# Kernel optimization log

Hardware: AMD Instinct MI355X
Metric: run time of the kernel (lower is better)

Reference implementation:

```python
import jax, jax.numpy as jnp
import numpy as np

N_QUBITS = 9
N_LAYERS = 4
EPS = 1e-5


def _apply_ry(state, wire, theta):
    # state: [N, 2**n] real; theta: [N] or scalar
    n = N_QUBITS
    N = state.shape[0]
    left, right = 2 ** wire, 2 ** (n - 1 - wire)
    s = state.reshape(N, left, 2, right)
    th = jnp.broadcast_to(jnp.asarray(theta, state.dtype), (N,))[:, None, None]
    c, si = jnp.cos(th / 2), jnp.sin(th / 2)
    a, b = s[:, :, 0, :], s[:, :, 1, :]
    out = jnp.stack([c * a - si * b, si * a + c * b], axis=2)
    return out.reshape(N, -1)


def _apply_cnot(state, ctrl, tgt):
    n = N_QUBITS
    N = state.shape[0]
    s = state.reshape((N,) + (2,) * n)
    ca, ta = ctrl + 1, tgt + 1
    sub = jnp.take(s, 1, axis=ca)          # control == 1 slice
    ta2 = ta - 1 if ta > ca else ta
    sub = jnp.flip(sub, axis=ta2)          # X on target
    idx = [slice(None)] * (n + 1)
    idx[ca] = 1
    s = s.at[tuple(idx)].set(sub)
    return s.reshape(N, -1)


def quantum_layer(inputs, q_weights):
    # inputs: [N, n_qubits] angles; q_weights: [n_layers, n_qubits]
    N = inputs.shape[0]
    state = jnp.zeros((N, 2 ** N_QUBITS), inputs.dtype).at[:, 0].set(1.0)
    for i in range(N_QUBITS):
        state = _apply_ry(state, i, inputs[:, i])
    for j in range(N_LAYERS):
        for i in range(N_QUBITS):
            state = _apply_cnot(state, i, (i + 1) % N_QUBITS)
        for i in range(N_QUBITS):
            state = _apply_ry(state, i, q_weights[j, i])
    probs = (state * state).reshape((N,) + (2,) * N_QUBITS)
    zs = []
    for i in range(N_QUBITS):
        axes = tuple(a for a in range(1, N_QUBITS + 1) if a != i + 1)
        p = probs.sum(axes)                # [N, 2]
        zs.append(p[:, 0] - p[:, 1])
    return jnp.stack(zs, axis=1)           # [N, n_qubits]


def _bn(x):
    mu = x.mean((0, 2, 3), keepdims=True)
    var = x.var((0, 2, 3), keepdims=True)
    return (x - mu) * jax.lax.rsqrt(var + EPS)


def _maxpool(x, kh, kw):
    return jax.lax.reduce_window(x, -jnp.inf, jax.lax.max,
                                 (1, 1, kh, kw), (1, 1, kh, kw), 'VALID')


def _conv(x, w):
    return jax.lax.conv_general_dilated(x, w, (1, 1), 'VALID',
                                        dimension_numbers=('NCHW', 'OIHW', 'NCHW'))


def _forward(x, w_conv1, w_conv2, w_conv3, q_weights, fc_w, fc_b):
    h = jax.nn.elu(_bn(_conv(x, w_conv1)))
    h = jnp.pad(h, ((0, 0), (0, 0), (0, 1), (16, 17)))     # ZeroPad2d(16,17,0,1)
    h = _maxpool(jax.nn.elu(_bn(_conv(h, w_conv2))), 2, 4)
    h = jnp.pad(h, ((0, 0), (0, 0), (4, 3), (2, 1)))       # ZeroPad2d(2,1,4,3)
    h = _maxpool(jax.nn.elu(_bn(_conv(h, w_conv3))), 2, 4)
    B, C = h.shape[0], h.shape[1]
    feats = h.reshape(B, C, -1)                            # [B, 32, 9]
    q = quantum_layer(feats.reshape(B * C, N_QUBITS), q_weights)
    q = q.reshape(B, C * N_QUBITS)                         # channel-major concat
    return q @ fc_w.T + fc_b


def setup_inputs() -> dict:
    key = jax.random.key(0)
    ks = jax.random.split(key, 7)
    return {
        'x': jax.random.normal(ks[0], (1024, 1, 4, 216), jnp.float32),
        'w_conv1': jax.random.normal(ks[1], (16, 1, 1, 64), jnp.float32) * 0.05,
        'w_conv2': jax.random.normal(ks[2], (32, 16, 2, 32), jnp.float32) * 0.05,
        'w_conv3': jax.random.normal(ks[3], (32, 32, 8, 4), jnp.float32) * 0.05,
        'q_weights': jax.random.uniform(ks[4], (N_LAYERS, N_QUBITS), jnp.float32, 0.0, 2 * np.pi),
        'fc_w': jax.random.normal(ks[5], (5, 32 * N_QUBITS), jnp.float32) * 0.05,
        'fc_b': jnp.zeros((5,), jnp.float32),
    }


def reference(x, w_conv1, w_conv2, w_conv3, q_weights, fc_w, fc_b):
    return _forward(x, w_conv1, w_conv2, w_conv3, q_weights, fc_w, fc_b)
```

## Files before the change

kernel.cpp:

```cpp
#include <hip/hip_runtime.h>
#include <math.h>

#define NB 1024
#define C1 16
#define H1 4
#define W1 153
#define WX 216
#define K1 64
#define C2 32
#define H2 4
#define W2 155
#define W192 192
#define PW2 38
#define C3 32
#define W3 38

typedef short short4v __attribute__((ext_vector_type(4)));
typedef short short8 __attribute__((ext_vector_type(8)));
typedef float f32x16 __attribute__((ext_vector_type(16)));

#define OFF_OUT1     0
#define OFF_A1H      10027008
#define OFF_A1L      16318464
#define OFF_W2PH     22609920
#define OFF_W2PL     22626304
#define OFF_W3PH     22642688
#define OFF_W3PL     22659072
#define OFF_UH       22675456
#define OFF_UL       22806528
#define OFF_POOL2RAW 22937600
#define OFF_A2H      25427968
#define OFF_A2L      27787264
#define OFF_FEATSRAW 30146560
#define OFF_QO       30441472
#define OFF_PART1    30736384
#define OFF_PART2    30867456
#define OFF_PART3    30998528
#define OFF_STATS1   31031296
#define OFF_STATS2   31031328
#define OFF_STATS3   31031392

__device__ __forceinline__ float eluf(float x){ return x > 0.f ? x : expm1f(x); }

__device__ __forceinline__ ushort bf16h(float x){
  unsigned u = __float_as_uint(x);
  unsigned r = u + 0x7fffu + ((u >> 16) & 1u);
  return (ushort)(r >> 16);
}
__device__ __forceinline__ float bf16f(ushort h){ return __uint_as_float(((unsigned)h) << 16); }

__device__ __forceinline__ short8 cat8(short4v a, short4v b){
  return __builtin_shufflevector(a, b, 0,1,2,3,4,5,6,7);
}

__global__ __launch_bounds__(256) void k_conv1s(const float* __restrict__ x,
                                                const float* __restrict__ w1,
                                                float* __restrict__ out1,
                                                float* __restrict__ part1){
  __shared__ float xr[4][WX];
  __shared__ float wl[C1*K1];
  int n = blockIdx.x, tid = threadIdx.x;
  for (int i = tid; i < 4*WX; i += 256) xr[i/WX][i%WX] = x[(size_t)n*4*WX + i];
  for (int i = tid; i < C1*K1; i += 256) wl[i] = w1[i];
  __syncthreads();
  int h = tid >> 6, lane = tid & 63;
  float acc[16][3];
  #pragma unroll
  for (int c = 0; c < 16; ++c){ acc[c][0]=0.f; acc[c][1]=0.f; acc[c][2]=0.f; }
  bool v2 = (lane + 128) < W1;
  for (int k = 0; k < 64; ++k){
    float x0 = xr[h][lane + k];
    float x1 = xr[h][lane + 64 + k];
    float x2 = v2 ? xr[h][lane + 128 + k] : 0.f;
    #pragma unroll
    for (int c = 0; c < 16; ++c){
      float wk = wl[c*64 + k];
      acc[c][0] += wk*x0; acc[c][1] += wk*x1; acc[c][2] += wk*x2;
    }
  }
  float ss[16], sq[16];
  #pragma unroll
  for (int c = 0; c < 16; ++c){
    float* ob = out1 + (((size_t)(n*16 + c)*4 + h))*W1;
    ob[lane] = acc[c][0];
    ob[lane + 64] = acc[c][1];
    if (v2) ob[lane + 128] = acc[c][2];
    ss[c] = acc[c][0] + acc[c][1] + acc[c][2];
    sq[c] = acc[c][0]*acc[c][0] + acc[c][1]*acc[c][1] + acc[c][2]*acc[c][2];
  }
  #pragma unroll
  for (int m = 1; m < 64; m <<= 1){
    #pragma unroll
    for (int c = 0; c < 16; ++c){ ss[c] += __shfl_xor(ss[c], m); sq[c] += __shfl_xor(sq[c], m); }
  }
  if (lane == 0){
    #pragma unroll
    for (int c = 0; c < 16; ++c){
      part1[((size_t)(n*4 + h)*16 + c)*2]     = ss[c];
      part1[((size_t)(n*4 + h)*16 + c)*2 + 1] = sq[c];
    }
  }
}

__global__ __launch_bounds__(256) void k_stats_finP(const float* __restrict__ part,
                                                    float* __restrict__ stats,
                                                    int C, int nblk, float inv){
  __shared__ float rs[256], rq[256];
  int c = blockIdx.x;
  float s = 0.f, q = 0.f;
  for (int b = threadIdx.x; b < nblk; b += 256){
    s += part[((size_t)b*C + c)*2];
    q += part[((size_t)b*C + c)*2 + 1];
  }
  rs[threadIdx.x] = s; rq[threadIdx.x] = q; __syncthreads();
  for (int st = 128; st > 0; st >>= 1){
    if (threadIdx.x < st){ rs[threadIdx.x] += rs[threadIdx.x+st]; rq[threadIdx.x] += rq[threadIdx.x+st]; }
    __syncthreads();
  }
  if (threadIdx.x == 0){
    float mean = rs[0]*inv;
    float var  = rq[0]*inv - mean*mean;
    stats[c*2]   = mean;
    stats[c*2+1] = rsqrtf(var + 1e-5f);
  }
}

__global__ __launch_bounds__(256) void k_bnelu1(const float* __restrict__ out1,
                                                const float* __restrict__ stats,
                                                ushort* __restrict__ a1h, ushort* __restrict__ a1l){
  __shared__ float xf[2448];
  __shared__ float st[32];
  int b = blockIdx.x;
  int n = b >> 2, h = b & 3;
  int tid = threadIdx.x;
  if (tid < 32) st[tid] = stats[tid];
  for (int i = tid; i < 2448; i += 256){
    int ci = i / 153, w = i - ci*153;
    xf[i] = out1[((size_t)(n*16 + ci)*4 + h)*W1 + w];
  }
  __syncthreads();
  for (int i = tid; i < 3072; i += 256){
    int w = i >> 4, ci = i & 15;
    float v = 0.f;
    int ws = w - 16;
    if ((unsigned)ws < (unsigned)W1){
      float xx = xf[ci*153 + ws];
      v = eluf((xx - st[ci*2])*st[ci*2+1]);
    }
    int ciS = ci ^ (((w >> 2) & 1) << 3);
    size_t o = (size_t)b*3072 + w*16 + ciS;
    ushort hs = bf16h(v);
    a1h[o] = hs;
    a1l[o] = bf16h(v - bf16f(hs));
  }
}

__global__ void k_cvtw(const float* __restrict__ w2, const float* __restrict__ w3,
                       ushort* __restrict__ w2ph, ushort* __restrict__ w2pl,
                       ushort* __restrict__ w3ph, ushort* __restrict__ w3pl){
  int idx = blockIdx.x*256 + threadIdx.x;
  if (idx < 32768){
    int ci = idx & 15; int co = (idx >> 4) & 31; int rk = idx >> 9;
    int r = rk >> 5, kw = rk & 31;
    float v = w2[((size_t)(co*16 + ci)*2 + r)*32 + kw];
    ushort hs = bf16h(v); float hf = bf16f(hs);
    w2ph[idx] = hs; w2pl[idx] = bf16h(v - hf);
  } else {
    int j = idx - 32768;
    int ci = j & 31; int co = (j >> 5) & 31; int rk = j >> 10;
    int r = rk >> 2, kw = rk & 3;
    float v = w3[((size_t)(co*32 + ci)*8 + r)*4 + kw];
    ushort hs = bf16h(v); float hf = bf16f(hs);
    w3ph[j] = hs; w3pl[j] = bf16h(v - hf);
  }
}

template<int HG, int PS>
__device__ __forceinline__ void conv2_body(const ushort* s_hi, const ushort* s_lo,
                                           const ushort* __restrict__ w2ph,
                                           const ushort* __restrict__ w2pl,
                                           float* __restrict__ pool2raw,
                                           float (*statW)[32][2],
                                           int n, int l31, int l5){
  constexpr int P0 = (PS == 0) ? 0 : (PS + 1);
  constexpr int NP = (PS == 0) ? 2 : 1;
  constexpr int NR = (HG == 0) ? 3 : 2;
  int e8 = l5*8;

  f32x16 acc[2][NP];
  #pragma unroll
  for (int lh = 0; lh < 2; ++lh)
    #pragma unroll
    for (int p = 0; p < NP; ++p)
      #pragma unroll
      for (int e = 0; e < 16; ++e) acc[lh][p][e] = 0.f;

  for (int kw = 0; kw < 32; ++kw){
    short8 Ah[2], Al[2];
    #pragma unroll
    for (int r = 0; r < 2; ++r){
      int widx = ((r*32 + kw)*32 + l31)*16 + e8;
      Ah[r] = *(const short8*)(w2ph + widx);
      Al[r] = *(const short8*)(w2pl + widx);
    }
    #pragma unroll
    for (int j = 0; j < NR; ++j){
      int rb = j*3072;
      short8 bh[NP], bl[NP];
      #pragma unroll
      for (int p = 0; p < NP; ++p){
        int pos = (P0 + p)*32 + l31 + kw;
        int off = rb + pos*16 + (e8 ^ (((pos >> 2) & 1) << 3));
        bh[p] = *(const short8*)(s_hi + off);
        bl[p] = *(const short8*)(s_lo + off);
      }
      #pragma unroll
      for (int lh = 0; lh < 2; ++lh){
        #pragma unroll
        for (int r = 0; r < 2; ++r){
          if (lh + r != j) continue;
          #pragma unroll
          for (int p = 0; p < NP; ++p){
            acc[lh][p] = __builtin_amdgcn_mfma_f32_32x32x16_bf16(Ah[r], bh[p], acc[lh][p], 0, 0, 0);
            acc[lh][p] = __builtin_amdgcn_mfma_f32_32x32x16_bf16(Ah[r], bl[p], acc[lh][p], 0, 0, 0);
            acc[lh][p] = __builtin_amdgcn_mfma_f32_32x32x16_bf16(Al[r], bh[p], acc[lh][p], 0, 0, 0);
          }
        }
      }
    }
  }

  {
    float sreg[16], qreg[16];
    #pragma unroll
    for (int e = 0; e < 16; ++e){ sreg[e] = 0.f; qreg[e] = 0.f; }
    #pragma unroll
    for (int lh = 0; lh < 2; ++lh){
      #pragma unroll
      for (int p = 0; p < NP; ++p){
        bool pv = ((P0 + p) < 4) || (l31 < 27);
        #pragma unroll
        for (int e = 0; e < 16; ++e){
          float v = pv ? acc[lh][p][e] : 0.f;
          sreg[e] += v; qreg[e] += v*v;
        }
      }
    }
    #pragma unroll
    for (int m = 1; m < 32; m <<= 1){
      #pragma unroll
      for (int e = 0; e < 16; ++e){
        sreg[e] += __shfl_xor(sreg[e], m);
        qreg[e] += __shfl_xor(qreg[e], m);
      }
    }
    if (l31 == 0){
      #pragma unroll
      for (int e = 0; e < 16; ++e){
        int co = (e & 3) + ((e >> 2) << 3) + (l5 << 2);
        statW[PS][co][0] = sreg[e];
        statW[PS][co][1] = qreg[e];
      }
    }
  }
  #pragma unroll
  for (int p = 0; p < NP; ++p){
    #pragma unroll
    for (int e = 0; e < 16; ++e){
      float m0 = fmaxf(acc[0][p][e], acc[1][p][e]);
      float v1 = fmaxf(m0, __shfl_xor(m0, 1));
      float v2m = fmaxf(v1, __shfl_xor(v1, 2));
      int pw = (P0 + p)*8 + (l31 >> 2);
      if ((l31 & 3) == 0 && pw < PW2){
        int co = (e & 3) + ((e >> 2) << 3) + (l5 << 2);
        pool2raw[(((size_t)n*2 + HG)*32 + co)*PW2 + pw] = v2m;
      }
    }
  }
}

__global__ __launch_bounds__(256, 4) void k_conv2f(const ushort* __restrict__ a1h,
                                                   const ushort* __restrict__ a1l,
                                                   const ushort* __restrict__ w2ph,
                                                   const ushort* __restrict__ w2pl,
                                                   float* __restrict__ pool2raw,
                                                   float* __restrict__ part2){
  __shared__ __align__(16) ushort s_hi[3*3072];
  __shared__ __align__(16) ushort s_lo[3*3072];
  __shared__ float statW[4][32][2];
  int b = blockIdx.x;
  int n = b >> 1, HG = b & 1;
  int tid = threadIdx.x;
  int nrows = HG ? 2 : 3;
  {
    const float4* gh = (const float4*)(a1h + ((size_t)n*4 + 2*HG)*3072);
    const float4* gl = (const float4*)(a1l + ((size_t)n*4 + 2*HG)*3072);
    float4* dh = (float4*)s_hi;
    float4* dl = (float4*)s_lo;
    int cnt = nrows*384;
    for (int i = tid; i < cnt; i += 256){ dh[i] = gh[i]; dl[i] = gl[i]; }
  }
  __syncthreads();
  int wv = tid >> 6, lane = tid & 63;
  int l5 = lane >> 5, l31 = lane & 31;
  int ps = (wv + b) & 3;
  if (HG == 0){
    switch (ps){
      case 0: conv2_body<0,0>(s_hi, s_lo, w2ph, w2pl, pool2raw, statW, n, l31, l5); break;
      case 1: conv2_body<0,1>(s_hi, s_lo, w2ph, w2pl, pool2raw, statW, n, l31, l5); break;
      case 2: conv2_body<0,2>(s_hi, s_lo, w2ph, w2pl, pool2raw, statW, n, l31, l5); break;
      default: conv2_body<0,3>(s_hi, s_lo, w2ph, w2pl, pool2raw, statW, n, l31, l5); break;
    }
  } else {
    switch (ps){
      case 0: conv2_body<1,0>(s_hi, s_lo, w2ph, w2pl, pool2raw, statW, n, l31, l5); break;
      case 1: conv2_body<1,1>(s_hi, s_lo, w2ph, w2pl, pool2raw, statW, n, l31, l5); break;
      case 2: conv2_body<1,2>(s_hi, s_lo, w2ph, w2pl, pool2raw, statW, n, l31, l5); break;
      default: conv2_body<1,3>(s_hi, s_lo, w2ph, w2pl, pool2raw, statW, n, l31, l5); break;
    }
  }
  __syncthreads();
  if (tid < 32){
    float s = statW[0][tid][0] + statW[1][tid][0] + statW[2][tid][0] + statW[3][tid][0];
    float q = statW[0][tid][1] + statW[1][tid][1] + statW[2][tid][1] + statW[3][tid][1];
    part2[(((size_t)n*2 + HG)*32 + tid)*2]     = s;
    part2[(((size_t)n*2 + HG)*32 + tid)*2 + 1] = q;
  }
}

__global__ __launch_bounds__(256) void k_bn2(const float* __restrict__ pool2raw,
                                             const float* __restrict__ stats,
                                             ushort* __restrict__ a2h, ushort* __restrict__ a2l){
  __shared__ float xf[1216];
  __shared__ float st[64];
  int b = blockIdx.x;
  int tid = threadIdx.x;
  if (tid < 64) st[tid] = stats[tid];
  for (int i = tid; i < 1216; i += 256) xf[i] = pool2raw[(size_t)b*1216 + i];
  __syncthreads();
  for (int i = tid; i < 2304; i += 256){
    int w = i >> 5, ci = i & 31;
    float v = 0.f;
    int pw = w - 2;
    if ((unsigned)pw < (unsigned)PW2)
      v = eluf((xf[ci*38 + pw] - st[ci*2])*st[ci*2+1]);
    int ciS = ci ^ (((w >> 1) & 7) << 2);
    size_t o = (size_t)b*2304 + w*32 + ciS;
    ushort hs = bf16h(v);
    a2h[o] = hs; a2l[o] = bf16h(v - bf16f(hs));
  }
}

__global__ __launch_bounds__(256, 2) void k_conv3f(const ushort* __restrict__ a2h,
                                                   const ushort* __restrict__ a2l,
                                                   const ushort* __restrict__ w3ph,
                                                   const ushort* __restrict__ w3pl,
                                                   float* __restrict__ featsraw,
                                                   float* __restrict__ part3){
  __shared__ __align__(16) ushort s3h[9216];
  __shared__ __align__(16) ushort s3l[9216];
  __shared__ float poolL3[4][32][12];
  __shared__ float statL3[4][32][2];
  int nb = blockIdx.x;
  int tid = threadIdx.x;
  {
    const float4* gh = (const float4*)(a2h + (size_t)nb*9216);
    const float4* gl = (const float4*)(a2l + (size_t)nb*9216);
    float4* dh = (float4*)s3h;
    float4* dl = (float4*)s3l;
    for (int i = tid; i < 1152; i += 256){ dh[i] = gh[i]; dl[i] = gl[i]; }
  }
  __syncthreads();
  int wave = tid >> 6, lane = tid & 63;
  int nh = wave >> 1, h = wave & 1;
  int l5 = lane >> 5, l31 = lane & 31;

  f32x16 acc[2];
  #pragma unroll
  for (int p = 0; p < 2; ++p)
    #pragma unroll
    for (int e = 0; e < 16; ++e) acc[p][e] = 0.f;

  #pragma unroll
  for (int ri = 0; ri < 2; ++ri){
    int r = (h == 0) ? (4 + ri) : (3 + ri);
    int rbase = (nh*2 + ri)*72*32;
    #pragma unroll
    for (int kw = 0; kw < 4; ++kw){
      #pragma unroll
      for (int ch = 0; ch < 2; ++ch){
        int widx = ((r*4 + kw)*32 + l31)*32 + ch*16 + l5*4;
        short8 Ah = cat8(*(const short4v*)(w3ph + widx), *(const short4v*)(w3ph + widx + 8));
        short8 Al = cat8(*(const short4v*)(w3pl + widx), *(const short4v*)(w3pl + widx + 8));
        short8 Bh[2], Bl[2];
        #pragma unroll
        for (int p = 0; p < 2; ++p){
          int pos = p*32 + l31 + kw;
          int sw = ((pos >> 1) & 7) << 2;
          int s0 = ch*16 + l5*4;
          int off0 = rbase + pos*32 + (s0 ^ sw);
          int off1 = rbase + pos*32 + ((s0 + 8) ^ sw);
          Bh[p] = cat8(*(const short4v*)(s3h + off0), *(const short4v*)(s3h + off1));
          Bl[p] = cat8(*(const short4v*)(s3l + off0), *(const short4v*)(s3l + off1));
        }
        #pragma unroll
        for (int p = 0; p < 2; ++p) acc[p] = __builtin_amdgcn_mfma_f32_32x32x16_bf16(Ah, Bh[p], acc[p], 0, 0, 0);
        #pragma unroll
        for (int p = 0; p < 2; ++p) acc[p] = __builtin_amdgcn_mfma_f32_32x32x16_bf16(Ah, Bl[p], acc[p], 0, 0, 0);
        #pragma unroll
        for (int p = 0; p < 2; ++p) acc[p] = __builtin_amdgcn_mfma_f32_32x32x16_bf16(Al, Bh[p], acc[p], 0, 0, 0);
      }
    }
  }

  {
    float sreg[16], qreg[16];
    #pragma unroll
    for (int e = 0; e < 16; ++e){ sreg[e] = 0.f; qreg[e] = 0.f; }
    #pragma unroll
    for (int p = 0; p < 2; ++p){
      bool pv = (p == 0) || (l31 < 6);
      #pragma unroll
      for (int e = 0; e < 16; ++e){
        float v = pv ? acc[p][e] : 0.f;
        sreg[e] += v; qreg[e] += v*v;
      }
    }
    #pragma unroll
    for (int m = 1; m < 32; m <<= 1){
      #pragma unroll
      for (int e = 0; e < 16; ++e){
        sreg[e] += __shfl_xor(sreg[e], m);
        qreg[e] += __shfl_xor(qreg[e], m);
      }
    }
    if (l31 == 0){
      #pragma unroll
      for (int e = 0; e < 16; ++e){
        int co = (e & 3) + ((e >> 2) << 3) + (l5 << 2);
        statL3[wave][co][0] = sreg[e];
        statL3[wave][co][1] = qreg[e];
      }
    }
  }
  #pragma unroll
  for (int p = 0; p < 2; ++p){
    #pragma unroll
    for (int e = 0; e < 16; ++e){
      float v = acc[p][e];
      float v1 = fmaxf(v, __shfl_xor(v, 1));
      float v2m = fmaxf(v1, __shfl_xor(v1, 2));
      int pw = p*8 + (l31 >> 2);
      if ((l31 & 3) == 0 && pw < 9){
        int co = (e & 3) + ((e >> 2) << 3) + (l5 << 2);
        poolL3[wave][co][pw] = v2m;
      }
    }
  }
  __syncthreads();
  for (int i = tid; i < 2*32*9; i += 256){
    int pw = i % 9; int t = i / 9; int co = t & 31; int nh2 = t >> 5;
    float v = fmaxf(poolL3[nh2*2][co][pw], poolL3[nh2*2+1][co][pw]);
    featsraw[((size_t)(nb*2 + nh2)*32 + co)*9 + pw] = v;
  }
  if (tid < 32){
    float s = 0.f, q = 0.f;
    #pragma unroll
    for (int wv = 0; wv < 4; ++wv){ s += statL3[wv][tid][0]; q += statL3[wv][tid][1]; }
    part3[((size_t)nb*32 + tid)*2]     = s;
    part3[((size_t)nb*32 + tid)*2 + 1] = q;
  }
}

__global__ __launch_bounds__(256) void k_buildU(const float* __restrict__ qw,
                                                ushort* __restrict__ Uh, ushort* __restrict__ Ul){
  __shared__ float wt[36][2];
  int tid = threadIdx.x;
  if (tid < 36){ float s, c; sincosf(qw[tid]*0.5f, &s, &c); wt[tid][0] = c; wt[tid][1] = s; }
  __syncthreads();
  int wid = tid >> 6, lane = tid & 63;
  int k = blockIdx.x*4 + wid;
  float v[8];
  #pragma unroll
  for (int r = 0; r < 8; ++r) v[r] = (lane*8 + r == k) ? 1.f : 0.f;

  for (int j = 0; j < 4; ++j){
    #pragma unroll
    for (int i = 0; i < 5; ++i){
      int cm = 32>>i, tm = 16>>i;
      bool flip = (lane & cm) != 0;
      #pragma unroll
      for (int r = 0; r < 8; ++r){
        float w = __shfl_xor(v[r], tm);
        v[r] = flip ? w : v[r];
      }
    }
    { bool flip = (lane & 1) != 0;
      #pragma unroll
      for (int r = 0; r < 4; ++r){ float a = v[r], bb = v[r+4]; v[r] = flip?bb:a; v[r+4] = flip?a:bb; } }
    { float t = v[4]; v[4] = v[6]; v[6] = t; t = v[5]; v[5] = v[7]; v[7] = t; }
    { float t = v[2]; v[2] = v[3]; v[3] = t; t = v[6]; v[6] = v[7]; v[7] = t; }
    #pragma unroll
    for (int r = 1; r < 8; r += 2) v[r] = __shfl_xor(v[r], 32);

    #pragma unroll
    for (int i = 0; i < 6; ++i){
      float c = wt[j*9+i][0], s = wt[j*9+i][1];
      int m = 32>>i;
      float sg = (lane & m) ? s : -s;
      #pragma unroll
      for (int r = 0; r < 8; ++r){
        float w = __shfl_xor(v[r], m);
        v[r] = c*v[r] + sg*w;
      }
    }
    { float c = wt[j*9+6][0], s = wt[j*9+6][1];
      #pragma unroll
      for (int r = 0; r < 4; ++r){ float a = v[r], bb = v[r+4]; v[r] = c*a - s*bb; v[r+4] = s*a + c*bb; } }
    { float c = wt[j*9+7][0], s = wt[j*9+7][1]; float a, bb;
      a=v[0]; bb=v[2]; v[0]=c*a-s*bb; v[2]=s*a+c*bb;
      a=v[1]; bb=v[3]; v[1]=c*a-s*bb; v[3]=s*a+c*bb;
      a=v[4]; bb=v[6]; v[4]=c*a-s*bb; v[6]=s*a+c*bb;
      a=v[5]; bb=v[7]; v[5]=c*a-s*bb; v[7]=s*a+c*bb; }
    { float c = wt[j*9+8][0], s = wt[j*9+8][1]; float a, bb;
      a=v[0]; bb=v[1]; v[0]=c*a-s*bb; v[1]=s*a+c*bb;
      a=v[2]; bb=v[3]; v[2]=c*a-s*bb; v[3]=s*a+c*bb;
      a=v[4]; bb=v[5]; v[4]=c*a-s*bb; v[5]=s*a+c*bb;
      a=v[6]; bb=v[7]; v[6]=c*a-s*bb; v[7]=s*a+c*bb; }
  }
  #pragma unroll
  for (int r = 0; r < 8; ++r){
    int s = lane*8 + r;
    int mf = s >> 5, r31 = s & 31;
    int addr = (((k >> 4)*16 + mf)*32 + r31)*16 + (k & 15);
    float f = v[r];
    ushort hi = bf16h(f);
    Uh[addr] = hi;
    Ul[addr] = bf16h(f - bf16f(hi));
  }
}

__global__ __launch_bounds__(256, 1) void k_qgemm(const float* __restrict__ featsraw,
                                                  const float* __restrict__ stats,
                                                  const ushort* __restrict__ Uh,
                                                  const ushort* __restrict__ Ul,
                                                  float* __restrict__ qo){
  __shared__ __align__(16) ushort BhL[32768];
  __shared__ __align__(16) ushort BlL[32768];
  __shared__ float angL[576];
  __shared__ float zred[4][64][9];
  int nb = blockIdx.x;
  int tid = threadIdx.x;
  for (int t = tid; t < 576; t += 256){
    float vr = featsraw[(size_t)nb*576 + t];
    int c = (t/9) & 31;
    angL[t] = 0.5f * eluf((vr - stats[c*2])*stats[c*2+1]);
  }
  __syncthreads();
  {
    int sm = tid >> 2, q = tid & 3;
    float tc[9], ts[9];
    #pragma unroll
    for (int i = 0; i < 9; ++i) sincosf(angL[sm*9 + i], &ts[i], &tc[i]);
    float Pc = ((q & 2) ? ts[0] : tc[0]) * ((q & 1) ? ts[1] : tc[1]);
    int swz = (sm >> 2) & 3;
    short4v* bh4 = (short4v*)BhL;
    short4v* bl4 = (short4v*)BlL;
    int j = 0;
    #pragma unroll
    for (int b2 = 0; b2 < 2; ++b2){ float p2 = Pc*(b2 ? ts[2] : tc[2]);
    #pragma unroll
    for (int b3 = 0; b3 < 2; ++b3){ float p3 = p2*(b3 ? ts[3] : tc[3]);
    #pragma unroll
    for (int b4 = 0; b4 < 2; ++b4){ float p4 = p3*(b4 ? ts[4] : tc[4]);
    #pragma unroll
    for (int b5 = 0; b5 < 2; ++b5){ float p5 = p4*(b5 ? ts[5] : tc[5]);
    #pragma unroll
    for (int b6 = 0; b6 < 2; ++b6){ float p6 = p5*(b6 ? ts[6] : tc[6]);
      float a0 = p6*tc[7]*tc[8];
      float a1 = p6*tc[7]*ts[8];
      float a2 = p6*ts[7]*tc[8];
      float a3 = p6*ts[7]*ts[8];
      ushort h0 = bf16h(a0), h1 = bf16h(a1), h2 = bf16h(a2), h3 = bf16h(a3);
      short4v hv; hv[0]=(short)h0; hv[1]=(short)h1; hv[2]=(short)h2; hv[3]=(short)h3;
      short4v lv; lv[0]=(short)bf16h(a0 - bf16f(h0)); lv[1]=(short)bf16h(a1 - bf16f(h1));
                  lv[2]=(short)bf16h(a2 - bf16f(h2)); lv[3]=(short)bf16h(a3 - bf16f(h3));
      int kk = q*128 + j;
      int kstep = kk >> 4;
      int g = (kk >> 2) & 3;
      int idx4 = (kstep*64 + sm)*4 + (g ^ swz);
      bh4[idx4] = hv; bl4[idx4] = lv;
      j += 4;
    }}}}}
  }
  __syncthreads();
  int wv = tid >> 6, lane = tid & 63, l5 = lane >> 5, l31 = lane & 31;
  f32x16 acc[4][2];
  #pragma unroll
  for (int jj = 0; jj < 4; ++jj)
    #pragma unroll
    for (int nf = 0; nf < 2; ++nf)
      #pragma unroll
      for (int e = 0; e < 16; ++e) acc[jj][nf][e] = 0.f;

  for (int kstep = 0; kstep < 32; ++kstep){
    short8 Bh[2], Bl[2];
    #pragma unroll
    for (int nf = 0; nf < 2; ++nf){
      int sm = nf*32 + l31;
      int base = (kstep*64 + sm)*16;
      int sz = ((sm >> 2) & 3) << 2;
      int e0 = (l5*4) ^ sz;
      int e1 = (l5*4 + 8) ^ sz;
      Bh[nf] = cat8(*(const short4v*)(BhL + base + e0), *(const short4v*)(BhL + base + e1));
      Bl[nf] = cat8(*(const short4v*)(BlL + base + e0), *(const short4v*)(BlL + base + e1));
    }
    #pragma unroll
    for (int jj = 0; jj < 4; ++jj){
      int mf = wv*4 + jj;
      const ushort* ah = Uh + ((kstep*16 + mf)*32 + l31)*16 + l5*4;
      const ushort* al = Ul + ((kstep*16 + mf)*32 + l31)*16 + l5*4;
      short8 Ah = cat8(*(const short4v*)ah, *(const short4v*)(ah + 8));
      short8 Al = cat8(*(const short4v*)al, *(const short4v*)(al + 8));
      acc[jj][0] = __builtin_amdgcn_mfma_f32_32x32x16_bf16(Ah, Bh[0], acc[jj][0], 0, 0, 0);
      acc[jj][1] = __builtin_amdgcn_mfma_f32_32x32x16_bf16(Ah, Bh[1], acc[jj][1], 0, 0, 0);
      acc[jj][0] = __builtin_amdgcn_mfma_f32_32x32x16_bf16(Ah, Bl[0], acc[jj][0], 0, 0, 0);
      acc[jj][1] = __builtin_amdgcn_mfma_f32_32x32x16_bf16(Ah, Bl[1], acc[jj][1], 0, 0, 0);
      acc[jj][0] = __builtin_amdgcn_mfma_f32_32x32x16_bf16(Al, Bh[0], acc[jj][0], 0, 0, 0);
      acc[jj][1] = __builtin_amdgcn_mfma_f32_32x32x16_bf16(Al, Bh[1], acc[jj][1], 0, 0, 0);
    }
  }
  float zz[2][9];
  #pragma unroll
  for (int nf = 0; nf < 2; ++nf)
    #pragma unroll
    for (int i = 0; i < 9; ++i) zz[nf][i] = 0.f;
  #pragma unroll
  for (int jj = 0; jj < 4; ++jj){
    int mf = wv*4 + jj;
    float sg0 = (mf & 8) ? -1.f : 1.f;
    float sg1 = (mf & 4) ? -1.f : 1.f;
    float sg2 = (mf & 2) ? -1.f : 1.f;
    float sg3 = (mf & 1) ? -1.f : 1.f;
    #pragma unroll
    for (int nf = 0; nf < 2; ++nf){
      float psum = 0.f, z4 = 0.f, z5 = 0.f, z7 = 0.f, z8 = 0.f;
      #pragma unroll
      for (int e = 0; e < 16; ++e){
        float qv = acc[jj][nf][e]*acc[jj][nf][e];
        psum += qv;
        z4 += ((e >> 3) & 1) ? -qv : qv;
        z5 += ((e >> 2) & 1) ? -qv : qv;
        z7 += ((e >> 1) & 1) ? -qv : qv;
        z8 += (e & 1) ? -qv : qv;
      }
      zz[nf][0] += sg0*psum; zz[nf][1] += sg1*psum;
      zz[nf][2] += sg2*psum; zz[nf][3] += sg3*psum;
      zz[nf][4] += z4; zz[nf][5] += z5;
      zz[nf][6] += l5 ? -psum : psum;
      zz[nf][7] += z7; zz[nf][8] += z8;
    }
  }
  #pragma unroll
  for (int nf = 0; nf < 2; ++nf)
    #pragma unroll
    for (int i = 0; i < 9; ++i) zz[nf][i] += __shfl_xor(zz[nf][i], 32);
  if (l5 == 0){
    #pragma unroll
    for (int nf = 0; nf < 2; ++nf)
      #pragma unroll
      for (int i = 0; i < 9; ++i) zred[wv][nf*32 + l31][i] = zz[nf][i];
  }
  __syncthreads();
  for (int t = tid; t < 576; t += 256){
    int sm = t / 9, i = t - sm*9;
    float s = zred[0][sm][i] + zred[1][sm][i] + zred[2][sm][i] + zred[3][sm][i];
    qo[(size_t)(nb*64 + sm)*9 + i] = s;
  }
}

__global__ void k_fc(const float* __restrict__ q, const float* __restrict__ fw,
                     const float* __restrict__ fb, float* __restrict__ out){
  int idx = blockIdx.x*256 + threadIdx.x;
  if (idx >= NB*5) return;
  int b = idx / 5, o = idx - b*5;
  const float* qr = q + (size_t)b*288;
  const float* wr = fw + (size_t)o*288;
  float s = 0.f;
  for (int j = 0; j < 288; ++j) s += qr[j]*wr[j];
  out[idx] = s + fb[o];
}

extern "C" void kernel_launch(void* const* d_in, const int* in_sizes, int n_in,
                              void* d_out, int out_size, void* d_ws, size_t ws_size,
                              hipStream_t stream){
  const float* x  = (const float*)d_in[0];
  const float* w1 = (const float*)d_in[1];
  const float* w2 = (const float*)d_in[2];
  const float* w3 = (const float*)d_in[3];
  const float* qw = (const float*)d_in[4];
  const float* fw = (const float*)d_in[5];
  const float* fb = (const float*)d_in[6];
  float* out = (float*)d_out;
  float* W = (float*)d_ws;

  float*  out1   = W + OFF_OUT1;
  ushort* a1h    = (ushort*)(W + OFF_A1H);
  ushort* a1l    = (ushort*)(W + OFF_A1L);
  ushort* w2ph   = (ushort*)(W + OFF_W2PH);
  ushort* w2pl   = (ushort*)(W + OFF_W2PL);
  ushort* w3ph   = (ushort*)(W + OFF_W3PH);
  ushort* w3pl   = (ushort*)(W + OFF_W3PL);
  ushort* uH     = (ushort*)(W + OFF_UH);
  ushort* uL     = (ushort*)(W + OFF_UL);
  float*  pool2raw = W + OFF_POOL2RAW;
  ushort* a2h    = (ushort*)(W + OFF_A2H);
  ushort* a2l    = (ushort*)(W + OFF_A2L);
  float*  featsraw = W + OFF_FEATSRAW;
  float*  qo     = W + OFF_QO;
  float*  part1  = W + OFF_PART1;
  float*  part2  = W + OFF_PART2;
  float*  part3  = W + OFF_PART3;
  float*  stats1 = W + OFF_STATS1;
  float*  stats2 = W + OFF_STATS2;
  float*  stats3 = W + OFF_STATS3;

  k_conv1s<<<NB, 256, 0, stream>>>(x, w1, out1, part1);
  k_stats_finP<<<16, 256, 0, stream>>>(part1, stats1, 16, NB*4, 1.f/((float)NB*H1*W1));
  k_bnelu1<<<NB*4, 256, 0, stream>>>(out1, stats1, a1h, a1l);
  k_cvtw<<<256, 256, 0, stream>>>(w2, w3, w2ph, w2pl, w3ph, w3pl);
  k_buildU<<<128, 256, 0, stream>>>(qw, uH, uL);
  k_conv2f<<<NB*2, 256, 0, stream>>>(a1h, a1l, w2ph, w2pl, pool2raw, part2);
  k_stats_finP<<<32, 256, 0, stream>>>(part2, stats2, 32, NB*2, 1.f/((float)NB*H2*W2));
  k_bn2<<<NB*2, 256, 0, stream>>>(pool2raw, stats2, a2h, a2l);
  k_conv3f<<<NB/2, 256, 0, stream>>>(a2h, a2l, w3ph, w3pl, featsraw, part3);
  k_stats_finP<<<32, 256, 0, stream>>>(part3, stats3, 32, NB/2, 1.f/((float)NB*2*W3));
  k_qgemm<<<NB/2, 256, 0, stream>>>(featsraw, stats3, uH, uL, qo);
  k_fc<<<20, 256, 0, stream>>>(qo, fw, fb, out);
}
```

Baseline: 316.3 us.

## Rework conv2 LDS swizzle and drop templated per-wave specializations

Changes the LDS swizzle of the bf16 activation buffer from a 1-bit XOR on 8-element halves to a 2-bit XOR on 4-element groups. The conv2 MFMA B-operand loads become pairs of 64-bit reads stitched with cat8, and the weight loads change to match. The eight template instantiations of conv2_body are replaced by one runtime-parameterized loop with np/nrows guards, and launch_bounds occupancy drops from 4 to 3. The goal is fewer LDS bank conflicts and less code bloat, at the cost of runtime branching, narrower loads and possibly lower occupancy.

Result: slower. 328.0 us (+3.7%).

```diff
diff --git a/kernel.cpp b/kernel.cpp
--- a/kernel.cpp
+++ b/kernel.cpp
@@ -147,7 +147,7 @@
       float xx = xf[ci*153 + ws];
       v = eluf((xx - st[ci*2])*st[ci*2+1]);
     }
-    int ciS = ci ^ (((w >> 2) & 1) << 3);
+    int ciS = ci ^ (((w >> 2) & 3) << 2);
     size_t o = (size_t)b*3072 + w*16 + ciS;
     ushort hs = bf16h(v);
     a1h[o] = hs;
@@ -175,111 +175,7 @@
   }
 }
 
-template<int HG, int PS>
-__device__ __forceinline__ void conv2_body(const ushort* s_hi, const ushort* s_lo,
-                                           const ushort* __restrict__ w2ph,
-                                           const ushort* __restrict__ w2pl,
-                                           float* __restrict__ pool2raw,
-                                           float (*statW)[32][2],
-                                           int n, int l31, int l5){
-  constexpr int P0 = (PS == 0) ? 0 : (PS + 1);
-  constexpr int NP = (PS == 0) ? 2 : 1;
-  constexpr int NR = (HG == 0) ? 3 : 2;
-  int e8 = l5*8;
-
-  f32x16 acc[2][NP];
-  #pragma unroll
-  for (int lh = 0; lh < 2; ++lh)
-    #pragma unroll
-    for (int p = 0; p < NP; ++p)
-      #pragma unroll
-      for (int e = 0; e < 16; ++e) acc[lh][p][e] = 0.f;
-
-  for (int kw = 0; kw < 32; ++kw){
-    short8 Ah[2], Al[2];
-    #pragma unroll
-    for (int r = 0; r < 2; ++r){
-      int widx = ((r*32 + kw)*32 + l31)*16 + e8;
-      Ah[r] = *(const short8*)(w2ph + widx);
-      Al[r] = *(const short8*)(w2pl + widx);
-    }
-    #pragma unroll
-    for (int j = 0; j < NR; ++j){
-      int rb = j*3072;
-      short8 bh[NP], bl[NP];
-      #pragma unroll
-      for (int p = 0; p < NP; ++p){
-        int pos = (P0 + p)*32 + l31 + kw;
-        int off = rb + pos*16 + (e8 ^ (((pos >> 2) & 1) << 3));
-        bh[p] = *(const short8*)(s_hi + off);
-        bl[p] = *(const short8*)(s_lo + off);
-      }
-      #pragma unroll
-      for (int lh = 0; lh < 2; ++lh){
-        #pragma unroll
-        for (int r = 0; r < 2; ++r){
-          if (lh + r != j) continue;
-          #pragma unroll
-          for (int p = 0; p < NP; ++p){
-            acc[lh][p] = __builtin_amdgcn_mfma_f32_32x32x16_bf16(Ah[r], bh[p], acc[lh][p], 0, 0, 0);
-            acc[lh][p] = __builtin_amdgcn_mfma_f32_32x32x16_bf16(Ah[r], bl[p], acc[lh][p], 0, 0, 0);
-            acc[lh][p] = __builtin_amdgcn_mfma_f32_32x32x16_bf16(Al[r], bh[p], acc[lh][p], 0, 0, 0);
-          }
-        }
-      }
-    }
-  }
-
-  {
-    float sreg[16], qreg[16];
-    #pragma unroll
-    for (int e = 0; e < 16; ++e){ sreg[e] = 0.f; qreg[e] = 0.f; }
-    #pragma unroll
-    for (int lh = 0; lh < 2; ++lh){
-      #pragma unroll
-      for (int p = 0; p < NP; ++p){
-        bool pv = ((P0 + p) < 4) || (l31 < 27);
-        #pragma unroll
-        for (int e = 0; e < 16; ++e){
-          float v = pv ? acc[lh][p][e] : 0.f;
-          sreg[e] += v; qreg[e] += v*v;
-        }
-      }
-    }
-    #pragma unroll
-    for (int m = 1; m < 32; m <<= 1){
-      #pragma unroll
-      for (int e = 0; e < 16; ++e){
-        sreg[e] += __shfl_xor(sreg[e], m);
-        qreg[e] += __shfl_xor(qreg[e], m);
-      }
-    }
-    if (l31 == 0){
-      #pragma unroll
-      for (int e = 0; e < 16; ++e){
-        int co = (e & 3) + ((e >> 2) << 3) + (l5 << 2);
-        statW[PS][co][0] = sreg[e];
-        statW[PS][co][1] = qreg[e];
-      }
-    }
-  }
-  #pragma unroll
-  for (int p = 0; p < NP; ++p){
-    #pragma unroll
-    for (int e = 0; e < 16; ++e){
-      float m0 = fmaxf(acc[0][p][e], acc[1][p][e]);
-      float v1 = fmaxf(m0, __shfl_xor(m0, 1));
-      float v2m = fmaxf(v1, __shfl_xor(v1, 2));
-      int pw = (P0 + p)*8 + (l31 >> 2);
-      if ((l31 & 3) == 0 && pw < PW2){
-        int co = (e & 3) + ((e >> 2) << 3) + (l5 << 2);
-        pool2raw[(((size_t)n*2 + HG)*32 + co)*PW2 + pw] = v2m;
-      }
-    }
-  }
-}
-
-__global__ __launch_bounds__(256, 4) void k_conv2f(const ushort* __restrict__ a1h,
+__global__ __launch_bounds__(256, 3) void k_conv2f(const ushort* __restrict__ a1h,
                                                    const ushort* __restrict__ a1l,
                                                    const ushort* __restrict__ w2ph,
                                                    const ushort* __restrict__ w2pl,
@@ -304,19 +200,106 @@
   int wv = tid >> 6, lane = tid & 63;
   int l5 = lane >> 5, l31 = lane & 31;
   int ps = (wv + b) & 3;
-  if (HG == 0){
-    switch (ps){
-      case 0: conv2_body<0,0>(s_hi, s_lo, w2ph, w2pl, pool2raw, statW, n, l31, l5); break;
-      case 1: conv2_body<0,1>(s_hi, s_lo, w2ph, w2pl, pool2raw, statW, n, l31, l5); break;
-      case 2: conv2_body<0,2>(s_hi, s_lo, w2ph, w2pl, pool2raw, statW, n, l31, l5); break;
-      default: conv2_body<0,3>(s_hi, s_lo, w2ph, w2pl, pool2raw, statW, n, l31, l5); break;
-    }
-  } else {
-    switch (ps){
-      case 0: conv2_body<1,0>(s_hi, s_lo, w2ph, w2pl, pool2raw, statW, n, l31, l5); break;
-      case 1: conv2_body<1,1>(s_hi, s_lo, w2ph, w2pl, pool2raw, statW, n, l31, l5); break;
-      case 2: conv2_body<1,2>(s_hi, s_lo, w2ph, w2pl, pool2raw, statW, n, l31, l5); break;
-      default: conv2_body<1,3>(s_hi, s_lo, w2ph, w2pl, pool2raw, statW, n, l31, l5); break;
+  int p0 = (ps == 0) ? 0 : (ps + 1);
+  int np = (ps == 0) ? 2 : 1;
+  int e4 = l5*4;
+
+  f32x16 acc[2][2];
+  #pragma unroll
+  for (int lh = 0; lh < 2; ++lh)
+    #pragma unroll
+    for (int p = 0; p < 2; ++p)
+      #pragma unroll
+      for (int e = 0; e < 16; ++e) acc[lh][p][e] = 0.f;
+
+  for (int kw = 0; kw < 32; ++kw){
+    short8 Ah[2], Al[2];
+    #pragma unroll
+    for (int r = 0; r < 2; ++r){
+      int widx = ((r*32 + kw)*32 + l31)*16 + e4;
+      Ah[r] = cat8(*(const short4v*)(w2ph + widx), *(const short4v*)(w2ph + widx + 8));
+      Al[r] = cat8(*(const short4v*)(w2pl + widx), *(const short4v*)(w2pl + widx + 8));
+    }
+    for (int j = 0; j < nrows; ++j){
+      int rb = j*3072;
+      short8 bh[2], bl[2];
+      #pragma unroll
+      for (int p = 0; p < 2; ++p){
+        if (p < np){
+          int pos = (p0 + p)*32 + l31 + kw;
+          int sw = ((pos >> 2) & 3) << 2;
+          int off0 = rb + pos*16 + (e4 ^ sw);
+          int off1 = rb + pos*16 + ((e4 + 8) ^ sw);
+          bh[p] = cat8(*(const short4v*)(s_hi + off0), *(const short4v*)(s_hi + off1));
+          bl[p] = cat8(*(const short4v*)(s_lo + off0), *(const short4v*)(s_lo + off1));
+        }
+      }
+      #pragma unroll
+      for (int lh = 0; lh < 2; ++lh){
+        #pragma unroll
+        for (int r = 0; r < 2; ++r){
+          if (lh + r == j){
+            #pragma unroll
+            for (int p = 0; p < 2; ++p){
+              if (p < np){
+                acc[lh][p] = __builtin_amdgcn_mfma_f32_32x32x16_bf16(Ah[r], bh[p], acc[lh][p], 0, 0, 0);
+                acc[lh][p] = __builtin_amdgcn_mfma_f32_32x32x16_bf16(Ah[r], bl[p], acc[lh][p], 0, 0, 0);
+                acc[lh][p] = __builtin_amdgcn_mfma_f32_32x32x16_bf16(Al[r], bh[p], acc[lh][p], 0, 0, 0);
+              }
+            }
+          }
+        }
+      }
+    }
+  }
+
+  {
+    float sreg[16], qreg[16];
+    #pragma unroll
+    for (int e = 0; e < 16; ++e){ sreg[e] = 0.f; qreg[e] = 0.f; }
+    #pragma unroll
+    for (int lh = 0; lh < 2; ++lh){
+      #pragma unroll
+      for (int p = 0; p < 2; ++p){
+        bool pv = (p < np) && (((p0 + p) < 4) || (l31 < 27));
+        #pragma unroll
+        for (int e = 0; e < 16; ++e){
+          float v = pv ? acc[lh][p][e] : 0.f;
+          sreg[e] += v; qreg[e] += v*v;
+        }
+      }
+    }
+    #pragma unroll
+    for (int m = 1; m < 32; m <<= 1){
+      #pragma unroll
+      for (int e = 0; e < 16; ++e){
+        sreg[e] += __shfl_xor(sreg[e], m);
+        qreg[e] += __shfl_xor(qreg[e], m);
+      }
+    }
+    if (l31 == 0){
+      #pragma unroll
+      for (int e = 0; e < 16; ++e){
+        int co = (e & 3) + ((e >> 2) << 3) + (l5 << 2);
+        statW[ps][co][0] = sreg[e];
+        statW[ps][co][1] = qreg[e];
+      }
+    }
+  }
+  #pragma unroll
+  for (int p = 0; p < 2; ++p){
+    if (p < np){
+      #pragma unroll
+      for (int e = 0; e < 16; ++e){
+        float m0 = fmaxf(acc[0][p][e], acc[1][p][e]);
+        float v1 = fmaxf(m0, __shfl_xor(m0, 1));
+        float v2m = fmaxf(v1, __shfl_xor(v1, 2));
+        int pw = (p0 + p)*8 + (l31 >> 2);
+        if ((l31 & 3) == 0 && pw < PW2){
+          int co = (e & 3) + ((e >> 2) << 3) + (l5 << 2);
+          pool2raw[(((size_t)n*2 + HG)*32 + co)*PW2 + pw] = v2m;
+        }
+      }
     }
   }
   __syncthreads();
```
